# Performance work log

Hardware: AMD Instinct MI355X
Metric: run time of the kernel (lower is better)

The kernel has to match this reference:

```python
import jax, jax.numpy as jnp
import numpy as np

HIDDEN = 4096
N_HEADS = 32
N_KV = 8
HEAD_DIM = HIDDEN // N_HEADS  # 128
ROT_DIM = int(HEAD_DIM * 0.5)  # partial_rotary_factor = 0.5 -> 64
ROPE_BASE = 1_000_000.0
EPS = 1e-6
T = 2048


def setup_inputs() -> dict:
    key = jax.random.key(0)
    k1, k2, k3, k4, k5 = jax.random.split(key, 5)
    qkv_out = (N_HEADS + 2 * N_KV) * HEAD_DIM  # 6144
    hidden_states = jax.random.normal(k1, (T, HIDDEN), dtype=jnp.float32)
    positions = jnp.arange(T, dtype=jnp.int32)
    w_qkv = jax.random.normal(k2, (HIDDEN, qkv_out), dtype=jnp.float32) * (HIDDEN ** -0.5)
    w_o = jax.random.normal(k3, (N_HEADS * HEAD_DIM, HIDDEN), dtype=jnp.float32) * ((N_HEADS * HEAD_DIM) ** -0.5)
    q_norm_w = jnp.ones((HEAD_DIM,), dtype=jnp.float32) + 0.01 * jax.random.normal(k4, (HEAD_DIM,), dtype=jnp.float32)
    k_norm_w = jnp.ones((HEAD_DIM,), dtype=jnp.float32) + 0.01 * jax.random.normal(k5, (HEAD_DIM,), dtype=jnp.float32)
    return {"hidden_states": hidden_states, "positions": positions,
            "w_qkv": w_qkv, "w_o": w_o, "q_norm_w": q_norm_w, "k_norm_w": k_norm_w}


def _rms_norm(x, w):
    # x: [T, H, D]; normalize over last dim
    var = jnp.mean(jnp.square(x), axis=-1, keepdims=True)
    return x * jax.lax.rsqrt(var + EPS) * w


def _apply_rope(x, positions):
    # neox-style rotary on first ROT_DIM dims of head_dim; rest passes through
    half = ROT_DIM // 2
    inv_freq = 1.0 / (ROPE_BASE ** (jnp.arange(0, ROT_DIM, 2, dtype=jnp.float32) / ROT_DIM))
    freqs = positions.astype(jnp.float32)[:, None] * inv_freq[None, :]  # [T, half]
    cos = jnp.cos(freqs)[:, None, :]  # [T, 1, half]
    sin = jnp.sin(freqs)[:, None, :]
    x_rot, x_pass = x[..., :ROT_DIM], x[..., ROT_DIM:]
    x1, x2 = x_rot[..., :half], x_rot[..., half:]
    rot = jnp.concatenate([x1 * cos - x2 * sin, x2 * cos + x1 * sin], axis=-1)
    return jnp.concatenate([rot, x_pass], axis=-1)


def reference(hidden_states, positions, w_qkv, w_o, q_norm_w, k_norm_w):
    q_size = N_HEADS * HEAD_DIM
    kv_size = N_KV * HEAD_DIM
    qkv = hidden_states @ w_qkv  # [T, q+2kv]
    q = qkv[:, :q_size].reshape(-1, N_HEADS, HEAD_DIM)
    k = qkv[:, q_size:q_size + kv_size].reshape(-1, N_KV, HEAD_DIM)
    v = qkv[:, q_size + kv_size:].reshape(-1, N_KV, HEAD_DIM)
    q = _rms_norm(q, q_norm_w)
    k = _rms_norm(k, k_norm_w)
    q = _apply_rope(q, positions)
    k = _apply_rope(k, positions)
    # GQA: repeat kv heads
    rep = N_HEADS // N_KV
    k = jnp.repeat(k, rep, axis=1)  # [T, H, D]
    v = jnp.repeat(v, rep, axis=1)
    scale = HEAD_DIM ** -0.5
    scores = jnp.einsum('thd,shd->hts', q, k) * scale  # [H, T, T]
    t = hidden_states.shape[0]
    causal = jnp.tril(jnp.ones((t, t), dtype=bool))
    scores = jnp.where(causal[None], scores, jnp.float32(-1e30))
    probs = jax.nn.softmax(scores, axis=-1)
    o = jnp.einsum('hts,shd->thd', probs, v).reshape(t, N_HEADS * HEAD_DIM)
    return o @ w_o
```

## Files before the change

### kernel.cpp

```cpp
#include <hip/hip_runtime.h>
#include <math.h>

#define HIDDEN 4096
#define QKV_N 6144
#define T_LEN 2048
#define HD 128
#define N_HEADS 32
#define N_KV 8
#define SCALE 0.08838834764831845f

typedef unsigned short u16;
typedef unsigned int u32;
typedef __attribute__((ext_vector_type(8))) short bf16x8;
typedef __attribute__((ext_vector_type(4))) float f32x4;

__device__ __forceinline__ u16 f2b(float x) {
  u32 u = __builtin_bit_cast(u32, x);
  u += 0x7fffu + ((u >> 16) & 1u);
  return (u16)(u >> 16);
}

typedef const __attribute__((address_space(1))) void* gas_ptr;
typedef __attribute__((address_space(3))) void* las_ptr;
__device__ __forceinline__ void gll16(const void* g, void* l) {
  __builtin_amdgcn_global_load_lds((gas_ptr)g, (las_ptr)l, 16, 0, 0);
}

__global__ __launch_bounds__(256) void cast_bf16_kernel(
    const float* __restrict__ in, u16* __restrict__ out) {
  const size_t i = ((size_t)blockIdx.x * 256 + threadIdx.x) * 4;
  f32x4 v = *(const f32x4*)(in + i);
  ushort4 o;
  o.x = f2b(v[0]); o.y = f2b(v[1]); o.z = f2b(v[2]); o.w = f2b(v[3]);
  *(ushort4*)(out + i) = o;
}

__global__ __launch_bounds__(256) void transpose_cast_kernel(
    const float* __restrict__ W, u16* __restrict__ WT, int K, int N) {
  __shared__ float t[32][33];
  const int n0 = blockIdx.x * 32, k0 = blockIdx.y * 32;
  const int c = threadIdx.x & 31;
  const int r0 = threadIdx.x >> 5;
#pragma unroll
  for (int j = 0; j < 4; ++j) {
    const int r = r0 + 8 * j;
    t[c][r] = W[(size_t)(k0 + r) * N + n0 + c];
  }
  __syncthreads();
#pragma unroll
  for (int j = 0; j < 4; ++j) {
    const int n = r0 + 8 * j;
    WT[(size_t)(n0 + n) * K + k0 + c] = f2b(t[n][c]);
  }
}

template <int BN>
__global__ __launch_bounds__(512, 2) void gemm256_kernel(
    const u16* __restrict__ A, const u16* __restrict__ BT,
    float* __restrict__ C, int M, int N, int K) {
  constexpr int WCOLS = BN / 4;
  constexpr int NF = WCOLS / 16;
  constexpr int BLOADS = BN / 128;
  __shared__ __align__(16) u16 As[2][2][256 * 32];
  __shared__ __align__(16) u16 Bs[2][2][BN * 32];

  const int tid = threadIdx.x;
  const int w = tid >> 6, l = tid & 63;
  const int wr = w >> 2, wc = w & 3;
  const int m = l & 15, g = l >> 4;
  const int bm = blockIdx.y * 256, bn = blockIdx.x * BN;
  const int NT = K >> 6;

  size_t gA[2]; int sA[2];
  size_t gB[2]; int sB[2];
#pragma unroll
  for (int i = 0; i < 2; ++i) {
    const int s = i * 512 + tid;
    const int r = s >> 2, o = s & 3;
    sA[i] = s * 8;
    gA[i] = (size_t)(bm + r) * K + (o ^ ((r >> 1) & 3)) * 8;
  }
#pragma unroll
  for (int i = 0; i < BLOADS; ++i) {
    const int s = i * 512 + tid;
    const int r = s >> 2, o = s & 3;
    sB[i] = s * 8;
    gB[i] = (size_t)(bn + r) * K + (o ^ ((r >> 1) & 3)) * 8;
  }

  const int foff = m * 32 + ((g ^ ((m >> 1) & 3)) * 8);
  const int abase = wr * 128 * 32;
  const int bbase = wc * WCOLS * 32;

#define STAGE_A(tile, kh)                                                      \
  {                                                                            \
    const size_t kofs = (size_t)(tile) * 64 + (kh) * 32;                       \
    u16* dst = &As[(tile) & 1][kh][0];                                         \
    gll16(A + gA[0] + kofs, dst + sA[0]);                                      \
    gll16(A + gA[1] + kofs, dst + sA[1]);                                      \
  }
#define STAGE_B(tile, kh)                                                      \
  {                                                                            \
    const size_t kofs = (size_t)(tile) * 64 + (kh) * 32;                       \
    u16* dst = &Bs[(tile) & 1][kh][0];                                         \
    gll16(BT + gB[0] + kofs, dst + sB[0]);                                     \
    if constexpr (BLOADS > 1) gll16(BT + gB[1] + kofs, dst + sB[1]);           \
  }
#define VM_COUNTED()                                                           \
  {                                                                            \
    if constexpr (BN == 256)                                                   \
      asm volatile("s_waitcnt vmcnt(4)" ::: "memory");                         \
    else                                                                       \
      asm volatile("s_waitcnt vmcnt(3)" ::: "memory");                         \
  }
#define STRETCH(kh, b, DO_STAGE, tn, VM)                                       \
  {                                                                            \
    bf16x8 af[8];                                                              \
    _Pragma("unroll") for (int fm = 0; fm < 8; ++fm)                           \
        af[fm] = *(const bf16x8*)(&As[b][kh][abase + fm * 512 + foff]);        \
    bf16x8 bf[NF];                                                             \
    _Pragma("unroll") for (int fn = 0; fn < NF; ++fn)                          \
        bf[fn] = *(const bf16x8*)(&Bs[b][kh][bbase + fn * 512 + foff]);        \
    if constexpr (DO_STAGE) { STAGE_A(tn, kh); STAGE_B(tn, kh); }              \
    __builtin_amdgcn_s_setprio(1);                                             \
    _Pragma("unroll") for (int fm = 0; fm < 8; ++fm)                           \
        _Pragma("unroll") for (int fn = 0; fn < NF; ++fn)                      \
        acc[fm][fn] = __builtin_amdgcn_mfma_f32_16x16x32_bf16(                 \
            af[fm], bf[fn], acc[fm][fn], 0, 0, 0);                             \
    __builtin_amdgcn_s_setprio(0);                                             \
    asm volatile("" ::: "memory");                                             \
    if constexpr ((VM) == 0) asm volatile("s_waitcnt vmcnt(0)" ::: "memory");  \
    if constexpr ((VM) == 1) VM_COUNTED();                                     \
    if constexpr ((VM) != 2) {                                                 \
      __builtin_amdgcn_s_barrier();                                            \
      asm volatile("" ::: "memory");                                           \
    }                                                                          \
  }

  f32x4 acc[8][NF];
#pragma unroll
  for (int i = 0; i < 8; ++i)
#pragma unroll
    for (int j = 0; j < NF; ++j) acc[i][j] = (f32x4){0.f, 0.f, 0.f, 0.f};

  STAGE_A(0, 0); STAGE_B(0, 0); STAGE_A(0, 1); STAGE_B(0, 1);
  VM_COUNTED();
  __builtin_amdgcn_s_barrier();
  asm volatile("" ::: "memory");

  for (int t = 0; t < NT - 1; ++t) {
    const int b = t & 1, tn = t + 1;
    STRETCH(0, b, true, tn, 1);
    STRETCH(1, b, true, tn, 1);
  }
  {
    const int b = (NT - 1) & 1;
    STRETCH(0, b, false, 0, 0);
    STRETCH(1, b, false, 0, 2);
  }
#undef STRETCH
#undef VM_COUNTED
#undef STAGE_B
#undef STAGE_A

#pragma unroll
  for (int fm = 0; fm < 8; ++fm) {
    const int row = bm + wr * 128 + fm * 16 + g * 4;
#pragma unroll
    for (int fn = 0; fn < NF; ++fn) {
      const int col = bn + wc * WCOLS + fn * 16 + m;
      float* cp = C + (size_t)row * N + col;
#pragma unroll
      for (int r = 0; r < 4; ++r) cp[(size_t)r * N] = acc[fm][fn][r];
    }
  }
}

__global__ __launch_bounds__(128) void normrope_pack_kernel(
    const float* __restrict__ qkv, const int* __restrict__ positions,
    const float* __restrict__ qw, const float* __restrict__ kw,
    u16* __restrict__ Qp, u16* __restrict__ Kp) {
  const int t = blockIdx.x;
  const int hh = blockIdx.y;
  const int d = threadIdx.x;
  const bool isq = hh < N_HEADS;
  const int col = isq ? hh * HD : HIDDEN + (hh - N_HEADS) * HD;
  const float* row = qkv + (size_t)t * QKV_N + col;
  const float* w = isq ? qw : kw;

  float x = row[d];
  float ss = x * x;
#pragma unroll
  for (int off = 32; off >= 1; off >>= 1) ss += __shfl_xor(ss, off);
  __shared__ float wsum[2];
  __shared__ float xs[128];
  if ((d & 63) == 0) wsum[d >> 6] = ss;
  __syncthreads();
  const float tot = wsum[0] + wsum[1];
  const float inv = rsqrtf(tot * (1.f / 128.f) + 1e-6f);
  const float xn = x * inv * w[d];
  xs[d] = xn;
  __syncthreads();

  float outv;
  if (d < 64) {
    const int idx = d & 31;
    const float invf = powf(1.0e6f, -(float)idx * (1.0f / 32.0f));
    const float fr = (float)positions[t] * invf;
    const float c = cosf(fr), s = sinf(fr);
    const float x1 = xs[idx], x2 = xs[idx + 32];
    outv = (d < 32) ? (x1 * c - x2 * s) : (x2 * c + x1 * s);
  } else {
    outv = xn;
  }
  if (isq) {
    Qp[((size_t)hh * T_LEN + t) * HD + d] = f2b(outv * SCALE);
  } else {
    Kp[((size_t)(hh - N_HEADS) * T_LEN + t) * HD + d] = f2b(outv);
  }
}

__global__ __launch_bounds__(256) void vtrans_kernel(
    const float* __restrict__ qkv, u16* __restrict__ Vtp) {
  __shared__ float tile[32][132];
  const int t0 = blockIdx.x * 32;
  const int kvh = blockIdx.y;
  const int tv = threadIdx.x >> 3;
  const int c0 = (threadIdx.x & 7) * 16;
  const float* src =
      qkv + (size_t)(t0 + tv) * QKV_N + (HIDDEN + 1024) + kvh * HD + c0;
#pragma unroll
  for (int u = 0; u < 4; ++u)
    *(f32x4*)&tile[tv][c0 + 4 * u] = *(const f32x4*)(src + 4 * u);
  __syncthreads();
  const int dd = threadIdx.x >> 1;
  const int half = threadIdx.x & 1;
  u16 buf[16];
#pragma unroll
  for (int p = 0; p < 16; ++p) buf[p] = f2b(tile[half * 16 + p][dd]);
  u16* dst = Vtp + ((size_t)kvh * HD + dd) * T_LEN + t0 + half * 16;
  *(uint4*)dst = *(uint4*)&buf[0];
  *(uint4*)(dst + 8) = *(uint4*)&buf[8];
}

__global__ __launch_bounds__(256, 3) void attn4_kernel(
    const u16* __restrict__ Qp, const u16* __restrict__ Kp,
    const u16* __restrict__ Vtp, u16* __restrict__ outB) {
  __shared__ __align__(16) u16 Qs[64 * 128];
  __shared__ __align__(16) u16 Ks[2 * 32 * 128];
  __shared__ __align__(16) u16 Vts[2 * 128 * 32];
  __shared__ __align__(16) u16 Plds[4 * 16 * 32];

  const int bx = blockIdx.x;
  const int h = blockIdx.y;
  const int kvh = h >> 2;
  const int tid = threadIdx.x;
  const int w = tid >> 6, l = tid & 63;
  const int g = l >> 4, m = l & 15;

  const u16* kbase = Kp + (size_t)kvh * T_LEN * HD;
  const u16* vbase = Vtp + (size_t)kvh * HD * T_LEN;
  u16* pl = Plds + w * 512;

#define STAGE_KV(jt, b)                                                        \
  {                                                                            \
    _Pragma("unroll") for (int p = 0; p < 2; ++p) {                            \
      const int krow = p * 16 + w * 4 + (l >> 4);                              \
      const int kg = (l & 15) ^ (krow & 7);                                    \
      gll16(kbase + (size_t)((jt) * 32 + krow) * 128 + kg * 8,                 \
            Ks + (b) * 4096 + p * 2048 + w * 512 + l * 8);                     \
      const int dv = p * 64 + w * 16 + (l >> 2);                               \
      const int vg = (l & 3) ^ ((dv >> 1) & 3);                                \
      gll16(vbase + (size_t)dv * T_LEN + (jt) * 32 + vg * 8,                   \
            Vts + (b) * 4096 + p * 2048 + w * 512 + l * 8);                    \
    }                                                                          \
  }

  for (int job = 0; job < 2; ++job) {
    const int qb = job ? bx : 31 - bx;
    const int t0 = qb * 64;
    const int NT = 2 * (qb + 1);

    {
      const u16* qbase = Qp + ((size_t)h * T_LEN + t0) * HD;
#pragma unroll
      for (int p = 0; p < 4; ++p) {
        const int row = p * 16 + w * 4 + (l >> 4);
        const int gr = (l & 15) ^ (row & 7);
        gll16(qbase + row * 128 + gr * 8, Qs + p * 2048 + w * 512 + l * 8);
      }
    }
    STAGE_KV(0, 0);
    __syncthreads();

    bf16x8 qf[4];
    {
      const u16* qr = Qs + (w * 16 + m) * 128;
#pragma unroll
      for (int kk = 0; kk < 4; ++kk)
        qf[kk] = *(const bf16x8*)(qr + (((kk * 4 + g) ^ (m & 7)) * 8));
    }

    f32x4 o[8];
#pragma unroll
    for (int n = 0; n < 8; ++n) o[n] = (f32x4){0.f, 0.f, 0.f, 0.f};
    float mrun = -1e30f, lrun = 0.f;

    for (int jt = 0; jt < NT; ++jt) {
      const int b = jt & 1;
      if (jt + 1 < NT) STAGE_KV(jt + 1, b ^ 1);

      f32x4 s[2];
      s[0] = (f32x4){0.f, 0.f, 0.f, 0.f};
      s[1] = (f32x4){0.f, 0.f, 0.f, 0.f};
      __builtin_amdgcn_s_setprio(1);
#pragma unroll
      for (int f = 0; f < 2; ++f) {
        const u16* kr = Ks + b * 4096 + (f * 16 + m) * 128;
#pragma unroll
        for (int kk = 0; kk < 4; ++kk) {
          bf16x8 kf = *(const bf16x8*)(kr + (((kk * 4 + g) ^ (m & 7)) * 8));
          s[f] =
              __builtin_amdgcn_mfma_f32_16x16x32_bf16(kf, qf[kk], s[f], 0, 0, 0);
        }
      }
      __builtin_amdgcn_s_setprio(0);

      if (jt >= NT - 2) {
        const int qg = t0 + w * 16 + m;
        const int kvb = jt * 32 + g * 4;
#pragma unroll
        for (int f = 0; f < 2; ++f)
#pragma unroll
          for (int r = 0; r < 4; ++r)
            if (kvb + f * 16 + r > qg) s[f][r] = -1e30f;
      }

      float pm = fmaxf(fmaxf(fmaxf(s[0][0], s[0][1]), fmaxf(s[0][2], s[0][3])),
                       fmaxf(fmaxf(s[1][0], s[1][1]), fmaxf(s[1][2], s[1][3])));
      pm = fmaxf(pm, __shfl_xor(pm, 16));
      pm = fmaxf(pm, __shfl_xor(pm, 32));
      if (!__all(pm <= mrun + 8.f)) {
        const float mn = fmaxf(mrun, pm);
        const float sc = __expf(mrun - mn);
        mrun = mn;
        lrun *= sc;
        f32x4 scr;
#pragma unroll
        for (int r = 0; r < 4; ++r) scr[r] = __shfl(sc, g * 4 + r);
#pragma unroll
        for (int n = 0; n < 8; ++n) o[n] *= scr;
      }
      float ps = 0.f;
#pragma unroll
      for (int f = 0; f < 2; ++f)
#pragma unroll
        for (int r = 0; r < 4; ++r) {
          s[f][r] = __expf(s[f][r] - mrun);
          ps += s[f][r];
        }
      ps += __shfl_xor(ps, 16);
      ps += __shfl_xor(ps, 32);
      lrun += ps;

      {
        const u32 a0 = (u32)f2b(s[0][0]) | ((u32)f2b(s[0][1]) << 16);
        const u32 a1 = (u32)f2b(s[0][2]) | ((u32)f2b(s[0][3]) << 16);
        const u32 b0 = (u32)f2b(s[1][0]) | ((u32)f2b(s[1][1]) << 16);
        const u32 b1 = (u32)f2b(s[1][2]) | ((u32)f2b(s[1][3]) << 16);
        *(uint2*)(pl + m * 32 + ((g ^ (m >> 1)) * 4)) = make_uint2(a0, a1);
        *(uint2*)(pl + m * 32 + (((g + 4) ^ (m >> 1)) * 4)) = make_uint2(b0, b1);
      }

      bf16x8 pa;
      {
        const uint2 lo =
            *(const uint2*)(pl + m * 32 + (((2 * g) ^ (m >> 1)) * 4));
        const uint2 hi =
            *(const uint2*)(pl + m * 32 + (((2 * g + 1) ^ (m >> 1)) * 4));
        union { u32 u[4]; bf16x8 v; } pu;
        pu.u[0] = lo.x; pu.u[1] = lo.y; pu.u[2] = hi.x; pu.u[3] = hi.y;
        pa = pu.v;
      }

      __builtin_amdgcn_s_setprio(1);
#pragma unroll
      for (int n = 0; n < 8; ++n) {
        const int dd = n * 16 + m;
        bf16x8 vf = *(const bf16x8*)(Vts + b * 4096 + dd * 32 +
                                     ((g ^ ((dd >> 1) & 3)) * 8));
        o[n] = __builtin_amdgcn_mfma_f32_16x16x32_bf16(pa, vf, o[n], 0, 0, 0);
      }
      __builtin_amdgcn_s_setprio(0);
      __syncthreads();
    }

    float li[4];
#pragma unroll
    for (int r = 0; r < 4; ++r) li[r] = 1.f / __shfl(lrun, g * 4 + r);
    u16* ob = outB + (size_t)(t0 + w * 16 + g * 4) * HIDDEN + h * HD + m;
#pragma unroll
    for (int n = 0; n < 8; ++n)
#pragma unroll
      for (int r = 0; r < 4; ++r)
        ob[(size_t)r * HIDDEN + n * 16] = f2b(o[n][r] * li[r]);
  }
#undef STAGE_KV
}

extern "C" void kernel_launch(void* const* d_in, const int* in_sizes, int n_in,
                              void* d_out, int out_size, void* d_ws,
                              size_t ws_size, hipStream_t stream) {
  const float* hidden = (const float*)d_in[0];
  const int* positions = (const int*)d_in[1];
  const float* w_qkv = (const float*)d_in[2];
  const float* w_o = (const float*)d_in[3];
  const float* q_norm_w = (const float*)d_in[4];
  const float* k_norm_w = (const float*)d_in[5];
  float* out = (float*)d_out;

  u16* hiddenB = (u16*)d_ws;
  u16* Qp = hiddenB;
  u16* wqkvT = hiddenB + (size_t)T_LEN * HIDDEN;
  u16* woT = wqkvT + (size_t)QKV_N * HIDDEN;
  float* qkv = (float*)(woT + (size_t)HIDDEN * HIDDEN);
  u16* attnB = (u16*)(qkv + (size_t)T_LEN * QKV_N);
  u16* Kp = attnB + (size_t)T_LEN * HIDDEN;
  u16* Vtp = Kp + (size_t)N_KV * T_LEN * HD;

  cast_bf16_kernel<<<(T_LEN * HIDDEN) / 1024, 256, 0, stream>>>(hidden, hiddenB);
  transpose_cast_kernel<<<dim3(QKV_N / 32, HIDDEN / 32), 256, 0, stream>>>(
      w_qkv, wqkvT, HIDDEN, QKV_N);
  transpose_cast_kernel<<<dim3(HIDDEN / 32, HIDDEN / 32), 256, 0, stream>>>(
      w_o, woT, HIDDEN, HIDDEN);

  gemm256_kernel<256><<<dim3(QKV_N / 256, T_LEN / 256), 512, 0, stream>>>(
      hiddenB, wqkvT, qkv, T_LEN, QKV_N, HIDDEN);
  normrope_pack_kernel<<<dim3(T_LEN, N_HEADS + N_KV), 128, 0, stream>>>(
      qkv, positions, q_norm_w, k_norm_w, Qp, Kp);
  vtrans_kernel<<<dim3(T_LEN / 32, N_KV), 256, 0, stream>>>(qkv, Vtp);
  attn4_kernel<<<dim3(16, N_HEADS), 256, 0, stream>>>(Qp, Kp, Vtp, attnB);
  gemm256_kernel<128><<<dim3(HIDDEN / 128, T_LEN / 256), 512, 0, stream>>>(
      attnB, woT, out, T_LEN, HIDDEN, HIDDEN);
}
```

Baseline: 348.0 us.

## Replace double-buffered GEMM pipeline with a three-slot ring of K=32 tiles

Restructures both GEMMs from a 2-stage double buffer of 64-wide K tiles (two 32-wide halves each) into a 3-slot ring buffer of 32-wide K tiles, prefetching two tiles ahead. Each iteration issues the load for tile t+2 while computing tile t, with one counted vmcnt wait and one barrier per 32-wide step. LDS use drops from 4 to 3 slots of 32-K tiles, and the prefetch distance and wait schedule change. The barrier count per K-element stays the same, so any gain depends on better latency hiding from the deeper prefetch.

Measured after the change: 431.8 us. 24.1% more time.

```diff
diff --git a/kernel.cpp b/kernel.cpp
--- a/kernel.cpp
+++ b/kernel.cpp
@@ -55,21 +55,24 @@
 }
 
 template <int BN>
-__global__ __launch_bounds__(512, 2) void gemm256_kernel(
+__global__ __launch_bounds__(512, 2) void gemm3_kernel(
     const u16* __restrict__ A, const u16* __restrict__ BT,
     float* __restrict__ C, int M, int N, int K) {
   constexpr int WCOLS = BN / 4;
   constexpr int NF = WCOLS / 16;
   constexpr int BLOADS = BN / 128;
-  __shared__ __align__(16) u16 As[2][2][256 * 32];
-  __shared__ __align__(16) u16 Bs[2][2][BN * 32];
+  constexpr int LPT = 2 + BLOADS;
+  constexpr int ABUF = 256 * 32;
+  constexpr int BBUF = BN * 32;
+  __shared__ __align__(16) u16 As[3 * ABUF];
+  __shared__ __align__(16) u16 Bs[3 * BBUF];
 
   const int tid = threadIdx.x;
   const int w = tid >> 6, l = tid & 63;
   const int wr = w >> 2, wc = w & 3;
   const int m = l & 15, g = l >> 4;
   const int bm = blockIdx.y * 256, bn = blockIdx.x * BN;
-  const int NT = K >> 6;
+  const int NT = K >> 5;
 
   size_t gA[2]; int sA[2];
   size_t gB[2]; int sB[2];
@@ -92,50 +95,21 @@
   const int abase = wr * 128 * 32;
   const int bbase = wc * WCOLS * 32;
 
-#define STAGE_A(tile, kh)                                                      \
+#define STAGE_TILE(tn, ao, bo)                                                 \
   {                                                                            \
-    const size_t kofs = (size_t)(tile) * 64 + (kh) * 32;                       \
-    u16* dst = &As[(tile) & 1][kh][0];                                         \
-    gll16(A + gA[0] + kofs, dst + sA[0]);                                      \
-    gll16(A + gA[1] + kofs, dst + sA[1]);                                      \
-  }
-#define STAGE_B(tile, kh)                                                      \
-  {                                                                            \
-    const size_t kofs = (size_t)(tile) * 64 + (kh) * 32;                       \
-    u16* dst = &Bs[(tile) & 1][kh][0];                                         \
-    gll16(BT + gB[0] + kofs, dst + sB[0]);                                     \
-    if constexpr (BLOADS > 1) gll16(BT + gB[1] + kofs, dst + sB[1]);           \
-  }
-#define VM_COUNTED()                                                           \
+    const size_t ko = (size_t)(tn) * 32;                                       \
+    gll16(A + gA[0] + ko, As + (ao) + sA[0]);                                  \
+    gll16(A + gA[1] + ko, As + (ao) + sA[1]);                                  \
+    gll16(BT + gB[0] + ko, Bs + (bo) + sB[0]);                                 \
+    if constexpr (BLOADS > 1) gll16(BT + gB[1] + ko, Bs + (bo) + sB[1]);       \
+  }
+#define VM_RING()                                                              \
   {                                                                            \
     if constexpr (BN == 256)                                                   \
       asm volatile("s_waitcnt vmcnt(4)" ::: "memory");                         \
     else                                                                       \
       asm volatile("s_waitcnt vmcnt(3)" ::: "memory");                         \
   }
-#define STRETCH(kh, b, DO_STAGE, tn, VM)                                       \
-  {                                                                            \
-    bf16x8 af[8];                                                              \
-    _Pragma("unroll") for (int fm = 0; fm < 8; ++fm)                           \
-        af[fm] = *(const bf16x8*)(&As[b][kh][abase + fm * 512 + foff]);        \
-    bf16x8 bf[NF];                                                             \
-    _Pragma("unroll") for (int fn = 0; fn < NF; ++fn)                          \
-        bf[fn] = *(const bf16x8*)(&Bs[b][kh][bbase + fn * 512 + foff]);        \
-    if constexpr (DO_STAGE) { STAGE_A(tn, kh); STAGE_B(tn, kh); }              \
-    __builtin_amdgcn_s_setprio(1);                                             \
-    _Pragma("unroll") for (int fm = 0; fm < 8; ++fm)                           \
-        _Pragma("unroll") for (int fn = 0; fn < NF; ++fn)                      \
-        acc[fm][fn] = __builtin_amdgcn_mfma_f32_16x16x32_bf16(                 \
-            af[fm], bf[fn], acc[fm][fn], 0, 0, 0);                             \
-    __builtin_amdgcn_s_setprio(0);                                             \
-    asm volatile("" ::: "memory");                                             \
-    if constexpr ((VM) == 0) asm volatile("s_waitcnt vmcnt(0)" ::: "memory");  \
-    if constexpr ((VM) == 1) VM_COUNTED();                                     \
-    if constexpr ((VM) != 2) {                                                 \
-      __builtin_amdgcn_s_barrier();                                            \
-      asm volatile("" ::: "memory");                                           \
-    }                                                                          \
-  }
 
   f32x4 acc[8][NF];
 #pragma unroll
@@ -143,25 +117,50 @@
 #pragma unroll
     for (int j = 0; j < NF; ++j) acc[i][j] = (f32x4){0.f, 0.f, 0.f, 0.f};
 
-  STAGE_A(0, 0); STAGE_B(0, 0); STAGE_A(0, 1); STAGE_B(0, 1);
-  VM_COUNTED();
+  STAGE_TILE(0, 0, 0);
+  STAGE_TILE(1, ABUF, BBUF);
+  VM_RING();
   __builtin_amdgcn_s_barrier();
   asm volatile("" ::: "memory");
 
-  for (int t = 0; t < NT - 1; ++t) {
-    const int b = t & 1, tn = t + 1;
-    STRETCH(0, b, true, tn, 1);
-    STRETCH(1, b, true, tn, 1);
-  }
-  {
-    const int b = (NT - 1) & 1;
-    STRETCH(0, b, false, 0, 0);
-    STRETCH(1, b, false, 0, 2);
-  }
-#undef STRETCH
-#undef VM_COUNTED
-#undef STAGE_B
-#undef STAGE_A
+  int a0 = 0, a1 = ABUF, a2 = 2 * ABUF;
+  int b0 = 0, b1 = BBUF, b2 = 2 * BBUF;
+
+  for (int t = 0; t < NT; ++t) {
+    bf16x8 af[8];
+#pragma unroll
+    for (int fm = 0; fm < 8; ++fm)
+      af[fm] = *(const bf16x8*)(&As[a0 + abase + fm * 512 + foff]);
+    if (t + 2 < NT) STAGE_TILE(t + 2, a2, b2);
+    bf16x8 bf[NF];
+#pragma unroll
+    for (int fn = 0; fn < NF; ++fn)
+      bf[fn] = *(const bf16x8*)(&Bs[b0 + bbase + fn * 512 + foff]);
+
+    __builtin_amdgcn_s_setprio(1);
+#pragma unroll
+    for (int fm = 0; fm < 8; ++fm)
+#pragma unroll
+      for (int fn = 0; fn < NF; ++fn)
+        acc[fm][fn] = __builtin_amdgcn_mfma_f32_16x16x32_bf16(
+            af[fm], bf[fn], acc[fm][fn], 0, 0, 0);
+    __builtin_amdgcn_s_setprio(0);
+    asm volatile("" ::: "memory");
+
+    if (t < NT - 2) {
+      VM_RING();
+      __builtin_amdgcn_s_barrier();
+      asm volatile("" ::: "memory");
+    } else if (t == NT - 2) {
+      asm volatile("s_waitcnt vmcnt(0)" ::: "memory");
+      __builtin_amdgcn_s_barrier();
+      asm volatile("" ::: "memory");
+    }
+    const int ta = a0; a0 = a1; a1 = a2; a2 = ta;
+    const int tb = b0; b0 = b1; b1 = b2; b2 = tb;
+  }
+#undef VM_RING
+#undef STAGE_TILE
 
 #pragma unroll
   for (int fm = 0; fm < 8; ++fm) {
@@ -434,12 +433,12 @@
   transpose_cast_kernel<<<dim3(HIDDEN / 32, HIDDEN / 32), 256, 0, stream>>>(
       w_o, woT, HIDDEN, HIDDEN);
 
-  gemm256_kernel<256><<<dim3(QKV_N / 256, T_LEN / 256), 512, 0, stream>>>(
+  gemm3_kernel<256><<<dim3(QKV_N / 256, T_LEN / 256), 512, 0, stream>>>(
       hiddenB, wqkvT, qkv, T_LEN, QKV_N, HIDDEN);
   normrope_pack_kernel<<<dim3(T_LEN, N_HEADS + N_KV), 128, 0, stream>>>(
       qkv, positions, q_norm_w, k_norm_w, Qp, Kp);
   vtrans_kernel<<<dim3(T_LEN / 32, N_KV), 256, 0, stream>>>(qkv, Vtp);
   attn4_kernel<<<dim3(16, N_HEADS), 256, 0, stream>>>(Qp, Kp, Vtp, attnB);
-  gemm256_kernel<128><<<dim3(HIDDEN / 128, T_LEN / 256), 512, 0, stream>>>(
+  gemm3_kernel<128><<<dim3(HIDDEN / 128, T_LEN / 256), 512, 0, stream>>>(
       attnB, woT, out, T_LEN, HIDDEN, HIDDEN);
 }
```
